# Optimization experiments

Hardware: AMD Instinct MI355X
Metric: run time of the kernel (lower is better)

## Reference

```python
import jax, jax.numpy as jnp
import numpy as np

B, S, H, NH, SPAN = 1, 2048, 768, 12, 512
D = H // NH
EPS = 1e-7
SCALE_FACTOR = 3  # 1 + len([c2p, p2c]) per DeBERTa


def setup_inputs() -> dict:
    key = jax.random.key(0)
    ks = jax.random.split(key, 10)
    r = lambda i, shape, s=0.02: jax.random.normal(ks[i], shape, jnp.float32) * s
    return dict(
        hidden_states=jax.random.normal(ks[0], (B, S, H), jnp.float32),
        attention_mask=jnp.ones((B, S), jnp.int32),
        Wq=r(1, (H, H)), bq=jnp.zeros((H,), jnp.float32),
        Wk=r(2, (H, H)), bk=jnp.zeros((H,), jnp.float32),
        Wv=r(3, (H, H)), bv=jnp.zeros((H,), jnp.float32),
        rel_embeddings=r(4, (2 * SPAN, H), 1.0),
        Wpk=r(5, (H, H)),
        Wpq=r(6, (H, H)), bpq=jnp.zeros((H,), jnp.float32),
        Wo=r(7, (H, H)), bo=jnp.zeros((H,), jnp.float32),
        ln_gamma=jnp.ones((H,), jnp.float32),
        ln_beta=jnp.zeros((H,), jnp.float32),
    )


def _heads(x):
    # [B,S,H] -> [B,NH,S,D]
    return x.reshape(B, S, NH, D).transpose(0, 2, 1, 3)


def reference(hidden_states, attention_mask, Wq, bq, Wk, bk, Wv, bv,
              rel_embeddings, Wpk, Wpq, bpq, Wo, bo, ln_gamma, ln_beta):
    q = _heads(hidden_states @ Wq + bq)
    k = _heads(hidden_states @ Wk + bk)
    v = _heads(hidden_states @ Wv + bv)
    scale = 1.0 / jnp.sqrt(jnp.asarray(D * SCALE_FACTOR, jnp.float32))

    # content-to-content
    scores = jnp.einsum('bhid,bhjd->bhij', q, k) * scale

    # relative positions: rel[i,j] = i - j
    ids = jnp.arange(S)
    rel = ids[:, None] - ids[None, :]                       # [S,S]

    pos_k = (rel_embeddings @ Wpk).reshape(2 * SPAN, NH, D)        # [2L,h,d]
    pos_q = (rel_embeddings @ Wpq + bpq).reshape(2 * SPAN, NH, D)  # [2L,h,d]

    # content-to-position: gather over clamped relative index
    c2p = jnp.einsum('bhid,lhd->bhil', q, pos_k) * scale    # [B,h,S,2L]
    c2p_idx = jnp.clip(rel + SPAN, 0, 2 * SPAN - 1)         # [S,S]
    c2p_att = c2p[:, :, ids[:, None], c2p_idx]              # [B,h,S,S]

    # position-to-content: gather then transpose (DeBERTa)
    p2c = jnp.einsum('bhjd,lhd->bhjl', k, pos_q) * scale    # [B,h,S,2L]
    p2c_idx = jnp.clip(-rel + SPAN, 0, 2 * SPAN - 1)        # [S,S]
    p2c_att = jnp.swapaxes(p2c[:, :, ids[:, None], p2c_idx], -1, -2)

    scores = scores + c2p_att + p2c_att

    mask4 = (attention_mask[:, None, None, :] * attention_mask[:, None, :, None]).astype(bool)
    scores = jnp.where(mask4, scores, jnp.finfo(scores.dtype).min)
    probs = jax.nn.softmax(scores, axis=-1)

    ctx = jnp.einsum('bhij,bhjd->bhid', probs, v).transpose(0, 2, 1, 3).reshape(B, S, H)

    # BertSelfOutput: dense + (dropout=identity) + residual + LayerNorm
    out = ctx @ Wo + bo + hidden_states
    mu = out.mean(-1, keepdims=True)
    var = out.var(-1, keepdims=True)
    return (out - mu) / jnp.sqrt(var + EPS) * ln_gamma + ln_beta
```

## Files before the change

### kernel.cpp

```cpp
#include <hip/hip_runtime.h>
#include <hip/hip_bf16.h>


typedef short v8s __attribute__((ext_vector_type(8)));
typedef short v4s __attribute__((ext_vector_type(4)));
typedef float v4f __attribute__((ext_vector_type(4)));

__device__ __forceinline__ float b2f(unsigned short u) {
    union { unsigned int i; float f; } v; v.i = ((unsigned int)u) << 16; return v.f;
}
__device__ __forceinline__ unsigned short f2b(float f) {
    union { float f; unsigned int i; } v; v.f = f;
    unsigned int x = v.i;
    return (unsigned short)((x + 0x7FFFu + ((x >> 16) & 1u)) >> 16);
}

#define SEQ 2048
#define HD  768
#define NH_ 12
#define DH  64

struct WtArgs { const float* src[6]; unsigned short* dst[6]; };
__global__ void prep_kernel(WtArgs args, const float* __restrict__ hs,
                            const float* __restrict__ rel,
                            const float* __restrict__ bq, const float* __restrict__ bk,
                            const float* __restrict__ bv, const float* __restrict__ bpq,
                            unsigned short* __restrict__ Xb, unsigned short* __restrict__ Rb,
                            float* __restrict__ bias3, float* __restrict__ bias2) {
    const int z = blockIdx.z;
    const int tx = threadIdx.x, ty = threadIdx.y;
    if (z < 6) {
        __shared__ float tile[32][33];
        const float* Sp = args.src[z];
        unsigned short* Dp = args.dst[z];
        const int bx = blockIdx.x * 32, by = blockIdx.y * 32;
#pragma unroll
        for (int r = 0; r < 32; r += 8) tile[ty + r][tx] = Sp[(by + ty + r) * HD + bx + tx];
        __syncthreads();
#pragma unroll
        for (int r = 0; r < 32; r += 8) Dp[(bx + ty + r) * HD + by + tx] = f2b(tile[tx][ty + r]);
    } else {
        const long n1 = (long)SEQ * HD;
        const long n2 = 1024l * HD;
        const long N = n1 + n2 + 3840;
        const long stride = 24l * 24 * 256;
        long i = ((long)blockIdx.y * 24 + blockIdx.x) * 256 + ty * 32 + tx;
        for (; i < N; i += stride) {
            if (i < n1) Xb[i] = f2b(hs[i]);
            else if (i < n1 + n2) Rb[i - n1] = f2b(rel[i - n1]);
            else {
                int j = (int)(i - n1 - n2);
                if (j < 768)        bias3[j] = bq[j];
                else if (j < 1536)  bias3[j] = bk[j - 768];
                else if (j < 2304)  bias3[j] = bv[j - 1536];
                else if (j < 3072)  bias2[j - 2304] = 0.0f;
                else                bias2[j - 2304] = bpq[j - 3072];
            }
        }
    }
}

template <int TM, int TN, int CTXA, int BIAS, int RESID, int OUTF32>
__device__ __forceinline__ void gemm_core(
    const unsigned short* __restrict__ A, int lda,
    const unsigned short* __restrict__ Bt, int ldb,
    void* __restrict__ Cv, int ldc,
    const float* __restrict__ bias, const float* __restrict__ resid,
    const float* __restrict__ opart, const float* __restrict__ lpart,
    int K, int m0, int n0, unsigned short* As, unsigned short* Bs) {
    constexpr int MT = TM / 32, NT = TN / 32;
    const int t = threadIdx.x;
    const int wave = t >> 6, lane = t & 63, quad = lane >> 4, l16 = lane & 15;
    const int wm = (wave & 1) * (TM / 2), wn = (wave >> 1) * (TN / 2);
    v4f acc[MT][NT];
    const v4f z4 = {0.f, 0.f, 0.f, 0.f};
#pragma unroll
    for (int i = 0; i < MT; i++)
#pragma unroll
        for (int j = 0; j < NT; j++) acc[i][j] = z4;

    const int arow = (TM == 128) ? (t >> 1) : (t >> 2);
    const int acol = (TM == 128) ? ((t & 1) * 32) : ((t & 3) * 16);
    const int brow = (TN == 128) ? (t >> 1) : (t >> 2);
    const int bcol = (TN == 128) ? ((t & 1) * 32) : ((t & 3) * 16);
    const unsigned short* ga = A + (long)(m0 + arow) * lda + acol;
    const unsigned short* gb = Bt + (long)(n0 + brow) * ldb + bcol;
    unsigned short* wa = &As[arow * 72 + acol];
    unsigned short* wb = &Bs[brow * 72 + bcol];

    for (int k0 = 0; k0 < K; k0 += 64) {
        __syncthreads();
        if constexpr (CTXA) {
            const int i = m0 + arow;
            const int h = k0 >> 6;
            float den = 0.f;
#pragma unroll
            for (int c = 0; c < 4; c++) den += lpart[((long)c * NH_ + h) * SEQ + i];
            const float inv = 1.0f / den;
            v8s pk0, pk1;
#pragma unroll
            for (int g = 0; g < 4; g++) {
                v4f s = z4;
#pragma unroll
                for (int c = 0; c < 4; c++)
                    s += *(const v4f*)(opart + (long)c * SEQ * HD + (long)i * HD + k0 + acol + g * 4);
#pragma unroll
                for (int u = 0; u < 4; u++) {
                    short v = (short)f2b(s[u] * inv);
                    if (g < 2) pk0[g * 4 + u] = v; else pk1[(g - 2) * 4 + u] = v;
                }
            }
            *(v8s*)wa = pk0; *(v8s*)(wa + 8) = pk1;
        } else if constexpr (TM == 128) {
            v8s a0 = *(const v8s*)(ga + k0);
            v8s a1 = *(const v8s*)(ga + k0 + 8);
            v8s a2 = *(const v8s*)(ga + k0 + 16);
            v8s a3 = *(const v8s*)(ga + k0 + 24);
            *(v8s*)(wa) = a0; *(v8s*)(wa + 8) = a1;
            *(v8s*)(wa + 16) = a2; *(v8s*)(wa + 24) = a3;
        } else {
            v8s a0 = *(const v8s*)(ga + k0);
            v8s a1 = *(const v8s*)(ga + k0 + 8);
            *(v8s*)(wa) = a0; *(v8s*)(wa + 8) = a1;
        }
        if constexpr (TN == 128) {
            v8s b0 = *(const v8s*)(gb + k0);
            v8s b1 = *(const v8s*)(gb + k0 + 8);
            v8s b2 = *(const v8s*)(gb + k0 + 16);
            v8s b3 = *(const v8s*)(gb + k0 + 24);
            *(v8s*)(wb) = b0; *(v8s*)(wb + 8) = b1;
            *(v8s*)(wb + 16) = b2; *(v8s*)(wb + 24) = b3;
        } else {
            v8s b0 = *(const v8s*)(gb + k0);
            v8s b1 = *(const v8s*)(gb + k0 + 8);
            *(v8s*)(wb) = b0; *(v8s*)(wb + 8) = b1;
        }
        __syncthreads();
#pragma unroll
        for (int ks = 0; ks < 2; ks++) {
            v8s af[MT], bf[NT];
#pragma unroll
            for (int mt = 0; mt < MT; mt++)
                af[mt] = *(const v8s*)&As[(wm + 16 * mt + l16) * 72 + ks * 32 + quad * 8];
#pragma unroll
            for (int nt = 0; nt < NT; nt++)
                bf[nt] = *(const v8s*)&Bs[(wn + 16 * nt + l16) * 72 + ks * 32 + quad * 8];
#pragma unroll
            for (int mt = 0; mt < MT; mt++)
#pragma unroll
                for (int nt = 0; nt < NT; nt++)
                    acc[mt][nt] = __builtin_amdgcn_mfma_f32_16x16x32_bf16(af[mt], bf[nt], acc[mt][nt], 0, 0, 0);
        }
    }
    float* Cf = (float*)Cv;
    unsigned short* Ch = (unsigned short*)Cv;
#pragma unroll
    for (int mt = 0; mt < MT; mt++) {
#pragma unroll
        for (int nt = 0; nt < NT; nt++) {
            const int gn = n0 + wn + 16 * nt + l16;
            float bv_ = 0.0f;
            if (BIAS) bv_ = bias[gn];
#pragma unroll
            for (int r = 0; r < 4; r++) {
                const int gm = m0 + wm + 16 * mt + quad * 4 + r;
                float v = acc[mt][nt][r];
                if (BIAS) v += bv_;
                if (RESID) v += resid[(long)gm * ldc + gn];
                if (OUTF32) Cf[(long)gm * ldc + gn] = v;
                else        Ch[(long)gm * ldc + gn] = f2b(v);
            }
        }
    }
}

__global__ __launch_bounds__(256) void gemm_qkvpos(
    const unsigned short* __restrict__ Xb, const unsigned short* __restrict__ Rb,
    const unsigned short* __restrict__ W3T, const unsigned short* __restrict__ Wp2T,
    const float* __restrict__ bias3, const float* __restrict__ bias2,
    unsigned short* __restrict__ qkv, unsigned short* __restrict__ pos2) {
    __shared__ unsigned short As[64 * 72];
    __shared__ unsigned short Bs[128 * 72];
    const int z = blockIdx.z;
    const int m0 = blockIdx.y * 64, n0 = blockIdx.x * 128;
    if (z < 3) {
        gemm_core<64, 128, 0, 1, 0, 0>(Xb, 768, W3T + (long)z * 768 * 768, 768,
                                       qkv + (long)z * 2048 * 768, 768, bias3 + z * 768,
                                       nullptr, nullptr, nullptr, 768, m0, n0, As, Bs);
    } else {
        if (blockIdx.y >= 16) return;
        const int w = z - 3;
        gemm_core<64, 128, 0, 1, 0, 0>(Rb, 768, Wp2T + (long)w * 768 * 768, 768,
                                       pos2 + (long)w * 1024 * 768, 768, bias2 + w * 768,
                                       nullptr, nullptr, nullptr, 768, m0, n0, As, Bs);
    }
}

__global__ __launch_bounds__(256) void gemm_band(
    const unsigned short* __restrict__ qkv, const unsigned short* __restrict__ pos2,
    unsigned short* __restrict__ c2p, unsigned short* __restrict__ p2c,
    const unsigned short* __restrict__ vsrc, unsigned short* __restrict__ vTs) {
    __shared__ unsigned short As[128 * 72];
    __shared__ unsigned short Bs[128 * 72];
    const int z = blockIdx.z;
    if (z < 24) {
        const unsigned short* A;
        const unsigned short* B;
        unsigned short* C;
        if (z < 12) {
            A = qkv + z * 64; B = pos2 + z * 64; C = c2p + (long)z * 2048 * 1024;
        } else {
            const int h = z - 12;
            A = qkv + 2048l * 768 + h * 64; B = pos2 + 1024l * 768 + h * 64;
            C = p2c + (long)h * 2048 * 1024;
        }
        gemm_core<128, 128, 0, 0, 0, 0>(A, 768, B, 768, C, 1024, nullptr, nullptr,
                                        nullptr, nullptr, 64,
                                        blockIdx.y * 128, blockIdx.x * 128, As, Bs);
    } else {
        unsigned short (*tile)[33] = (unsigned short(*)[33])As;
        const int b = blockIdx.y * 8 + blockIdx.x;
        const int tx = threadIdx.x & 31, ty = threadIdx.x >> 5;
        for (int tid = b; tid < 1536; tid += 128) {
            const int cx = (tid % 24) * 32;
            const int ry = (tid / 24) * 32;
            __syncthreads();
#pragma unroll
            for (int r = 0; r < 32; r += 8)
                tile[ty + r][tx] = vsrc[(long)(ry + ty + r) * HD + cx + tx];
            __syncthreads();
#pragma unroll
            for (int r = 0; r < 32; r += 8)
                vTs[(long)(cx + ty + r) * SEQ + ry + tx] = tile[tx][ty + r];
        }
    }
}

__global__ __launch_bounds__(256) void gemm_out(
    const float* __restrict__ opart, const float* __restrict__ lpart,
    const unsigned short* __restrict__ WoT,
    const float* __restrict__ bo, const float* __restrict__ hidden,
    float* __restrict__ out_pre) {
    __shared__ unsigned short As[64 * 72];
    __shared__ unsigned short Bs[64 * 72];
    gemm_core<64, 64, 1, 1, 1, 1>(nullptr, 768, WoT, 768, out_pre, 768, bo, hidden,
                                  opart, lpart, 768,
                                  blockIdx.y * 64, blockIdx.x * 64, As, Bs);
}

__device__ __forceinline__ void stage_window(const unsigned short* __restrict__ row,
                                             int D0, v8s& w0, v8s& w1) {
    if (D0 <= 0) {
        unsigned short v = row[0];
#pragma unroll
        for (int u = 0; u < 8; u++) { w0[u] = (short)v; w1[u] = (short)v; }
    } else if (D0 - 15 >= 1023) {
        unsigned short v = row[1023];
#pragma unroll
        for (int u = 0; u < 8; u++) { w0[u] = (short)v; w1[u] = (short)v; }
    } else if (D0 <= 1023 && D0 - 15 >= 0) {
        v8s x = *(const v8s*)(row + D0 - 7);
        v8s y = *(const v8s*)(row + D0 - 15);
#pragma unroll
        for (int u = 0; u < 8; u++) { w0[u] = x[7 - u]; w1[u] = y[7 - u]; }
    } else {
#pragma unroll
        for (int u = 0; u < 16; u++) {
            int d = D0 - u; d = d < 0 ? 0 : (d > 1023 ? 1023 : d);
            short v = (short)row[d];
            if (u < 8) w0[u] = v; else w1[u - 8] = v;
        }
    }
}

__global__ __launch_bounds__(256, 4) void flash_kernel(
    const unsigned short* __restrict__ qb, const unsigned short* __restrict__ kb,
    const unsigned short* __restrict__ vT, const unsigned short* __restrict__ c2p,
    const unsigned short* __restrict__ p2c, float* __restrict__ opart,
    float* __restrict__ lpart) {
    __shared__ unsigned short Kl[64 * 72];
    __shared__ unsigned short Vl[64 * 72];
    __shared__ unsigned short Pw[64 * 72];
    __shared__ unsigned short CwPl[64 * 72];
    const int h = blockIdx.y;
    const int i0 = blockIdx.x * 64;
    const int jc = blockIdx.z;
    const int jbase = jc * 512;
    const int t = threadIdx.x;
    const int wave = t >> 6, lane = t & 63, quad = lane >> 4, l16 = lane & 15;
    const float scale = 0.07216878364870322f;
    const v4f z4 = {0.f, 0.f, 0.f, 0.f};

    v8s qf[2];
    {
        const unsigned short* qp = qb + (long)(i0 + wave * 16 + l16) * HD + h * DH + quad * 8;
        qf[0] = *(const v8s*)qp;
        qf[1] = *(const v8s*)(qp + 32);
    }
    float l_lane[4] = {0.f, 0.f, 0.f, 0.f};
    v4f o_acc[4];
#pragma unroll
    for (int nt = 0; nt < 4; nt++) o_acc[nt] = z4;

    const int srow = t >> 2, scoff = (t & 3) * 16;
    const unsigned short* kbase = kb + (long)srow * HD + h * DH + scoff;
    const unsigned short* vbase = vT + (long)(h * DH + srow) * SEQ + scoff + jbase;
    unsigned short* wk = &Kl[srow * 72 + scoff];
    unsigned short* wv = &Vl[srow * 72 + scoff];
    unsigned short* wc = &CwPl[srow * 72 + scoff];
    unsigned short* wp = &Pw[srow * 72 + scoff];
    const unsigned short* c2prow = c2p + ((long)h * SEQ + i0 + srow) * 1024;
    const unsigned short* p2cb = p2c + (long)h * SEQ * 1024;

    v8s k0v, k1v, v0v, v1v, cw0, cw1, pw0, pw1;
    auto load_tile = [&](int j0l) {
        k0v = *(const v8s*)(kbase + (long)(jbase + j0l) * HD);
        k1v = *(const v8s*)(kbase + (long)(jbase + j0l) * HD + 8);
        v0v = *(const v8s*)(vbase + j0l);
        v1v = *(const v8s*)(vbase + j0l + 8);
        stage_window(c2prow, (i0 + srow) - (jbase + j0l) - scoff + 512, cw0, cw1);
        stage_window(p2cb + (long)(jbase + j0l + srow) * 1024,
                     (jbase + j0l + srow) - i0 - scoff + 512, pw0, pw1);
    };
    load_tile(0);

    for (int tt = 0; tt < 8; tt++) {
        __syncthreads();
        *(v8s*)wk = k0v; *(v8s*)(wk + 8) = k1v;
        *(v8s*)wv = v0v; *(v8s*)(wv + 8) = v1v;
        *(v8s*)wc = cw0; *(v8s*)(wc + 8) = cw1;
        *(v8s*)wp = pw0; *(v8s*)(wp + 8) = pw1;
        if (tt + 1 < 8) load_tile((tt + 1) * 64);
        __syncthreads();

        v4f s[4] = {z4, z4, z4, z4};
#pragma unroll
        for (int ks = 0; ks < 2; ks++)
#pragma unroll
            for (int nt = 0; nt < 4; nt++) {
                v8s bf = *(const v8s*)&Kl[(16 * nt + l16) * 72 + ks * 32 + quad * 8];
                s[nt] = __builtin_amdgcn_mfma_f32_16x16x32_bf16(qf[ks], bf, s[nt], 0, 0, 0);
            }
        float sm[4][4];
#pragma unroll
        for (int nt = 0; nt < 4; nt++) {
            v4s p4 = *(const v4s*)&Pw[(nt * 16 + l16) * 72 + wave * 16 + quad * 4];
#pragma unroll
            for (int r = 0; r < 4; r++) {
                float c2pv = b2f(CwPl[(wave * 16 + quad * 4 + r) * 72 + nt * 16 + l16]);
                float p = __expf((s[nt][r] + c2pv + b2f((unsigned short)p4[r])) * scale);
                sm[nt][r] = p;
                l_lane[r] += p;
            }
        }
#pragma unroll
        for (int nt = 0; nt < 4; nt++)
#pragma unroll
            for (int r = 0; r < 4; r++)
                CwPl[(wave * 16 + quad * 4 + r) * 72 + nt * 16 + l16] = f2b(sm[nt][r]);
        asm volatile("s_waitcnt lgkmcnt(0)" ::: "memory");
#pragma unroll
        for (int ks = 0; ks < 2; ks++) {
            v8s pf = *(const v8s*)&CwPl[(wave * 16 + l16) * 72 + ks * 32 + quad * 8];
#pragma unroll
            for (int nt = 0; nt < 4; nt++) {
                v8s vf = *(const v8s*)&Vl[(16 * nt + l16) * 72 + ks * 32 + quad * 8];
                o_acc[nt] = __builtin_amdgcn_mfma_f32_16x16x32_bf16(pf, vf, o_acc[nt], 0, 0, 0);
            }
        }
    }
    float* op = opart + (long)jc * SEQ * HD;
#pragma unroll
    for (int nt = 0; nt < 4; nt++) {
        const int d = nt * 16 + l16;
#pragma unroll
        for (int r = 0; r < 4; r++) {
            const int i = i0 + wave * 16 + quad * 4 + r;
            op[(long)i * HD + h * DH + d] = o_acc[nt][r];
        }
    }
#pragma unroll
    for (int r = 0; r < 4; r++) {
        float l = l_lane[r];
#pragma unroll
        for (int off = 1; off < 16; off <<= 1) l += __shfl_xor(l, off);
        l_lane[r] = l;
    }
    if (l16 == 0) {
#pragma unroll
        for (int r = 0; r < 4; r++) {
            const int i = i0 + wave * 16 + quad * 4 + r;
            lpart[((long)jc * NH_ + h) * SEQ + i] = l_lane[r];
        }
    }
}

__global__ __launch_bounds__(256) void ln_kernel(const float* __restrict__ x,
                                                 const float* __restrict__ gamma,
                                                 const float* __restrict__ beta,
                                                 float* __restrict__ out) {
    const int row = blockIdx.x;
    const int t = threadIdx.x;
    const float* xr = x + (long)row * HD;
    float v0 = xr[t], v1 = xr[t + 256], v2 = xr[t + 512];
    float s = v0 + v1 + v2;
    float ss = v0 * v0 + v1 * v1 + v2 * v2;
#pragma unroll
    for (int off = 1; off < 64; off <<= 1) { s += __shfl_xor(s, off); ss += __shfl_xor(ss, off); }
    __shared__ float red[8];
    const int wave = t >> 6;
    if ((t & 63) == 0) { red[wave] = s; red[wave + 4] = ss; }
    __syncthreads();
    float S = red[0] + red[1] + red[2] + red[3];
    float SS = red[4] + red[5] + red[6] + red[7];
    const float inv = 1.0f / 768.0f;
    float mu = S * inv;
    float var = SS * inv - mu * mu;
    float rstd = rsqrtf(var + 1e-7f);
    float* orow = out + (long)row * HD;
    orow[t]       = (v0 - mu) * rstd * gamma[t]       + beta[t];
    orow[t + 256] = (v1 - mu) * rstd * gamma[t + 256] + beta[t + 256];
    orow[t + 512] = (v2 - mu) * rstd * gamma[t + 512] + beta[t + 512];
}

extern "C" void kernel_launch(void* const* d_in, const int* in_sizes, int n_in,
                              void* d_out, int out_size, void* d_ws, size_t ws_size,
                              hipStream_t stream) {
    const float* hidden = (const float*)d_in[0];
    const float* Wq  = (const float*)d_in[2];
    const float* bq  = (const float*)d_in[3];
    const float* Wk  = (const float*)d_in[4];
    const float* bk  = (const float*)d_in[5];
    const float* Wv  = (const float*)d_in[6];
    const float* bv  = (const float*)d_in[7];
    const float* rel = (const float*)d_in[8];
    const float* Wpk = (const float*)d_in[9];
    const float* Wpq = (const float*)d_in[10];
    const float* bpq = (const float*)d_in[11];
    const float* Wo  = (const float*)d_in[12];
    const float* bo  = (const float*)d_in[13];
    const float* gamma = (const float*)d_in[14];
    const float* beta  = (const float*)d_in[15];

    char* ws = (char*)d_ws;
    size_t off = 0;
    auto alloc = [&](size_t bytes) -> char* { char* p = ws + off; off += bytes; return p; };
    unsigned short* Xb   = (unsigned short*)alloc(2048ul * 768 * 2);
    unsigned short* Rb   = (unsigned short*)alloc(1024ul * 768 * 2);
    unsigned short* W3T  = (unsigned short*)alloc(3ul * 768 * 768 * 2);
    unsigned short* WoT  = (unsigned short*)alloc(768ul * 768 * 2);
    unsigned short* Wp2T = (unsigned short*)alloc(2ul * 768 * 768 * 2);
    float*          bias3 = (float*)alloc(2304 * 4);
    float*          bias2 = (float*)alloc(1536 * 4);
    unsigned short* qkv  = (unsigned short*)alloc(3ul * 2048 * 768 * 2);
    unsigned short* vTs  = (unsigned short*)alloc(768ul * 2048 * 2);
    unsigned short* pos2 = (unsigned short*)alloc(2ul * 1024 * 768 * 2);
    unsigned short* c2p  = (unsigned short*)alloc(12ul * 2048 * 1024 * 2);
    unsigned short* p2c  = (unsigned short*)alloc(12ul * 2048 * 1024 * 2);
    float*          out_pre = (float*)alloc(2048ul * 768 * 4);
    float*          opart   = (float*)alloc(4ul * 2048 * 768 * 4);
    float*          lpart   = (float*)alloc(4ul * 12 * 2048 * 4);
    (void)ws_size;

    WtArgs wa;
    wa.src[0] = Wq;  wa.dst[0] = W3T;
    wa.src[1] = Wk;  wa.dst[1] = W3T + 768 * 768;
    wa.src[2] = Wv;  wa.dst[2] = W3T + 2 * 768 * 768;
    wa.src[3] = Wo;  wa.dst[3] = WoT;
    wa.src[4] = Wpk; wa.dst[4] = Wp2T;
    wa.src[5] = Wpq; wa.dst[5] = Wp2T + 768 * 768;
    prep_kernel<<<dim3(24, 24, 7), dim3(32, 8), 0, stream>>>(
        wa, hidden, rel, bq, bk, bv, bpq, Xb, Rb, bias3, bias2);

    gemm_qkvpos<<<dim3(6, 32, 5), 256, 0, stream>>>(Xb, Rb, W3T, Wp2T, bias3, bias2, qkv, pos2);
    gemm_band<<<dim3(8, 16, 25), 256, 0, stream>>>(qkv, pos2, c2p, p2c,
                                                   qkv + 2ul * 2048 * 768, vTs);
    flash_kernel<<<dim3(32, 12, 4), 256, 0, stream>>>(qkv, qkv + 2048ul * 768, vTs, c2p, p2c,
                                                      opart, lpart);
    gemm_out<<<dim3(12, 32), 256, 0, stream>>>(opart, lpart, WoT, bo, hidden, out_pre);
    ln_kernel<<<2048, 256, 0, stream>>>(out_pre, gamma, beta, (float*)d_out);
}
```

Measured before the change: 261.4 us.

## Fuse all stages into a persistent megakernel with software grid barriers

Replaces six separate kernel launches with one persistent kernel of 768 blocks that walks through each stage in a grid-stride loop and separates stages with an atomic-counter grid barrier. Flash partial outputs are now stored as bf16 instead of fp32, and the partial-sum combine moves into a separate elementwise pass that writes a bf16 ctx buffer for the output GEMM. The aim is to cut launch overhead, inter-kernel gaps and partial-output traffic. In exchange it relies on all 768 blocks being co-resident, since otherwise the barrier deadlocks, and it adds barrier latency plus some precision loss in the partials.

```diff
diff --git a/kernel.cpp b/kernel.cpp
--- a/kernel.cpp
+++ b/kernel.cpp
@@ -19,54 +19,44 @@
 #define HD  768
 #define NH_ 12
 #define DH  64
-
-struct WtArgs { const float* src[6]; unsigned short* dst[6]; };
-__global__ void prep_kernel(WtArgs args, const float* __restrict__ hs,
-                            const float* __restrict__ rel,
-                            const float* __restrict__ bq, const float* __restrict__ bk,
-                            const float* __restrict__ bv, const float* __restrict__ bpq,
-                            unsigned short* __restrict__ Xb, unsigned short* __restrict__ Rb,
-                            float* __restrict__ bias3, float* __restrict__ bias2) {
-    const int z = blockIdx.z;
-    const int tx = threadIdx.x, ty = threadIdx.y;
-    if (z < 6) {
-        __shared__ float tile[32][33];
-        const float* Sp = args.src[z];
-        unsigned short* Dp = args.dst[z];
-        const int bx = blockIdx.x * 32, by = blockIdx.y * 32;
-#pragma unroll
-        for (int r = 0; r < 32; r += 8) tile[ty + r][tx] = Sp[(by + ty + r) * HD + bx + tx];
-        __syncthreads();
-#pragma unroll
-        for (int r = 0; r < 32; r += 8) Dp[(bx + ty + r) * HD + by + tx] = f2b(tile[tx][ty + r]);
-    } else {
-        const long n1 = (long)SEQ * HD;
-        const long n2 = 1024l * HD;
-        const long N = n1 + n2 + 3840;
-        const long stride = 24l * 24 * 256;
-        long i = ((long)blockIdx.y * 24 + blockIdx.x) * 256 + ty * 32 + tx;
-        for (; i < N; i += stride) {
-            if (i < n1) Xb[i] = f2b(hs[i]);
-            else if (i < n1 + n2) Rb[i - n1] = f2b(rel[i - n1]);
-            else {
-                int j = (int)(i - n1 - n2);
-                if (j < 768)        bias3[j] = bq[j];
-                else if (j < 1536)  bias3[j] = bk[j - 768];
-                else if (j < 2304)  bias3[j] = bv[j - 1536];
-                else if (j < 3072)  bias2[j - 2304] = 0.0f;
-                else                bias2[j - 2304] = bpq[j - 3072];
-            }
-        }
-    }
-}
-
-template <int TM, int TN, int CTXA, int BIAS, int RESID, int OUTF32>
+#define NBLK 768
+
+struct MegaArgs {
+    const float *hs, *rel;
+    const float *Wq, *bq, *Wk, *bk, *Wv, *bv, *Wpk, *Wpq, *bpq, *Wo, *bo, *gamma, *beta;
+    unsigned short *Xb, *Rb, *W3T, *WoT, *Wp2T, *qkv, *vTs, *pos2, *c2p, *p2c, *ctx, *opart;
+    float *bias3, *bias2, *out_pre, *lpart, *outp;
+    unsigned* bar;
+};
+
+__device__ __forceinline__ void grid_sync(unsigned* bar) {
+    __syncthreads();
+    if (threadIdx.x == 0) {
+        unsigned* cnt = bar;
+        unsigned* gen = bar + 64;
+        unsigned g = __hip_atomic_load(gen, __ATOMIC_RELAXED, __HIP_MEMORY_SCOPE_AGENT);
+        unsigned a = __hip_atomic_fetch_add(cnt, 1u, __ATOMIC_ACQ_REL, __HIP_MEMORY_SCOPE_AGENT);
+        if (a == NBLK - 1) {
+            __hip_atomic_store(cnt, 0u, __ATOMIC_RELAXED, __HIP_MEMORY_SCOPE_AGENT);
+            __hip_atomic_store(gen, g + 1u, __ATOMIC_RELEASE, __HIP_MEMORY_SCOPE_AGENT);
+        } else {
+            unsigned cur;
+            do {
+                __builtin_amdgcn_s_sleep(16);
+                cur = __hip_atomic_load(gen, __ATOMIC_RELAXED, __HIP_MEMORY_SCOPE_AGENT);
+            } while (cur == g);
+            (void)__hip_atomic_load(gen, __ATOMIC_ACQUIRE, __HIP_MEMORY_SCOPE_AGENT);
+        }
+    }
+    __syncthreads();
+}
+
+template <int TM, int TN, int BIAS, int RESID, int OUTF32>
 __device__ __forceinline__ void gemm_core(
     const unsigned short* __restrict__ A, int lda,
     const unsigned short* __restrict__ Bt, int ldb,
     void* __restrict__ Cv, int ldc,
     const float* __restrict__ bias, const float* __restrict__ resid,
-    const float* __restrict__ opart, const float* __restrict__ lpart,
     int K, int m0, int n0, unsigned short* As, unsigned short* Bs) {
     constexpr int MT = TM / 32, NT = TN / 32;
     const int t = threadIdx.x;
@@ -90,28 +80,7 @@
 
     for (int k0 = 0; k0 < K; k0 += 64) {
         __syncthreads();
-        if constexpr (CTXA) {
-            const int i = m0 + arow;
-            const int h = k0 >> 6;
-            float den = 0.f;
-#pragma unroll
-            for (int c = 0; c < 4; c++) den += lpart[((long)c * NH_ + h) * SEQ + i];
-            const float inv = 1.0f / den;
-            v8s pk0, pk1;
-#pragma unroll
-            for (int g = 0; g < 4; g++) {
-                v4f s = z4;
-#pragma unroll
-                for (int c = 0; c < 4; c++)
-                    s += *(const v4f*)(opart + (long)c * SEQ * HD + (long)i * HD + k0 + acol + g * 4);
-#pragma unroll
-                for (int u = 0; u < 4; u++) {
-                    short v = (short)f2b(s[u] * inv);
-                    if (g < 2) pk0[g * 4 + u] = v; else pk1[(g - 2) * 4 + u] = v;
-                }
-            }
-            *(v8s*)wa = pk0; *(v8s*)(wa + 8) = pk1;
-        } else if constexpr (TM == 128) {
+        if constexpr (TM == 128) {
             v8s a0 = *(const v8s*)(ga + k0);
             v8s a1 = *(const v8s*)(ga + k0 + 8);
             v8s a2 = *(const v8s*)(ga + k0 + 16);
@@ -174,80 +143,6 @@
     }
 }
 
-__global__ __launch_bounds__(256) void gemm_qkvpos(
-    const unsigned short* __restrict__ Xb, const unsigned short* __restrict__ Rb,
-    const unsigned short* __restrict__ W3T, const unsigned short* __restrict__ Wp2T,
-    const float* __restrict__ bias3, const float* __restrict__ bias2,
-    unsigned short* __restrict__ qkv, unsigned short* __restrict__ pos2) {
-    __shared__ unsigned short As[64 * 72];
-    __shared__ unsigned short Bs[128 * 72];
-    const int z = blockIdx.z;
-    const int m0 = blockIdx.y * 64, n0 = blockIdx.x * 128;
-    if (z < 3) {
-        gemm_core<64, 128, 0, 1, 0, 0>(Xb, 768, W3T + (long)z * 768 * 768, 768,
-                                       qkv + (long)z * 2048 * 768, 768, bias3 + z * 768,
-                                       nullptr, nullptr, nullptr, 768, m0, n0, As, Bs);
-    } else {
-        if (blockIdx.y >= 16) return;
-        const int w = z - 3;
-        gemm_core<64, 128, 0, 1, 0, 0>(Rb, 768, Wp2T + (long)w * 768 * 768, 768,
-                                       pos2 + (long)w * 1024 * 768, 768, bias2 + w * 768,
-                                       nullptr, nullptr, nullptr, 768, m0, n0, As, Bs);
-    }
-}
-
-__global__ __launch_bounds__(256) void gemm_band(
-    const unsigned short* __restrict__ qkv, const unsigned short* __restrict__ pos2,
-    unsigned short* __restrict__ c2p, unsigned short* __restrict__ p2c,
-    const unsigned short* __restrict__ vsrc, unsigned short* __restrict__ vTs) {
-    __shared__ unsigned short As[128 * 72];
-    __shared__ unsigned short Bs[128 * 72];
-    const int z = blockIdx.z;
-    if (z < 24) {
-        const unsigned short* A;
-        const unsigned short* B;
-        unsigned short* C;
-        if (z < 12) {
-            A = qkv + z * 64; B = pos2 + z * 64; C = c2p + (long)z * 2048 * 1024;
-        } else {
-            const int h = z - 12;
-            A = qkv + 2048l * 768 + h * 64; B = pos2 + 1024l * 768 + h * 64;
-            C = p2c + (long)h * 2048 * 1024;
-        }
-        gemm_core<128, 128, 0, 0, 0, 0>(A, 768, B, 768, C, 1024, nullptr, nullptr,
-                                        nullptr, nullptr, 64,
-                                        blockIdx.y * 128, blockIdx.x * 128, As, Bs);
-    } else {
-        unsigned short (*tile)[33] = (unsigned short(*)[33])As;
-        const int b = blockIdx.y * 8 + blockIdx.x;
-        const int tx = threadIdx.x & 31, ty = threadIdx.x >> 5;
-        for (int tid = b; tid < 1536; tid += 128) {
-            const int cx = (tid % 24) * 32;
-            const int ry = (tid / 24) * 32;
-            __syncthreads();
-#pragma unroll
-            for (int r = 0; r < 32; r += 8)
-                tile[ty + r][tx] = vsrc[(long)(ry + ty + r) * HD + cx + tx];
-            __syncthreads();
-#pragma unroll
-            for (int r = 0; r < 32; r += 8)
-                vTs[(long)(cx + ty + r) * SEQ + ry + tx] = tile[tx][ty + r];
-        }
-    }
-}
-
-__global__ __launch_bounds__(256) void gemm_out(
-    const float* __restrict__ opart, const float* __restrict__ lpart,
-    const unsigned short* __restrict__ WoT,
-    const float* __restrict__ bo, const float* __restrict__ hidden,
-    float* __restrict__ out_pre) {
-    __shared__ unsigned short As[64 * 72];
-    __shared__ unsigned short Bs[64 * 72];
-    gemm_core<64, 64, 1, 1, 1, 1>(nullptr, 768, WoT, 768, out_pre, 768, bo, hidden,
-                                  opart, lpart, 768,
-                                  blockIdx.y * 64, blockIdx.x * 64, As, Bs);
-}
-
 __device__ __forceinline__ void stage_window(const unsigned short* __restrict__ row,
                                              int D0, v8s& w0, v8s& w1) {
     if (D0 <= 0) {
@@ -273,23 +168,19 @@
     }
 }
 
-__global__ __launch_bounds__(256, 4) void flash_kernel(
-    const unsigned short* __restrict__ qb, const unsigned short* __restrict__ kb,
-    const unsigned short* __restrict__ vT, const unsigned short* __restrict__ c2p,
-    const unsigned short* __restrict__ p2c, float* __restrict__ opart,
-    float* __restrict__ lpart) {
-    __shared__ unsigned short Kl[64 * 72];
-    __shared__ unsigned short Vl[64 * 72];
-    __shared__ unsigned short Pw[64 * 72];
-    __shared__ unsigned short CwPl[64 * 72];
-    const int h = blockIdx.y;
-    const int i0 = blockIdx.x * 64;
-    const int jc = blockIdx.z;
+__device__ __forceinline__ void flash_unit(const MegaArgs& a, int i0, int h, int jc,
+                                           unsigned short* smem) {
+    unsigned short* Kl = smem;
+    unsigned short* Vl = smem + 4608;
+    unsigned short* Pw = smem + 9216;
+    unsigned short* CwPl = smem + 13824;
     const int jbase = jc * 512;
     const int t = threadIdx.x;
     const int wave = t >> 6, lane = t & 63, quad = lane >> 4, l16 = lane & 15;
     const float scale = 0.07216878364870322f;
     const v4f z4 = {0.f, 0.f, 0.f, 0.f};
+    const unsigned short* qb = a.qkv;
+    const unsigned short* kb = a.qkv + (long)SEQ * HD;
 
     v8s qf[2];
     {
@@ -304,13 +195,13 @@
 
     const int srow = t >> 2, scoff = (t & 3) * 16;
     const unsigned short* kbase = kb + (long)srow * HD + h * DH + scoff;
-    const unsigned short* vbase = vT + (long)(h * DH + srow) * SEQ + scoff + jbase;
+    const unsigned short* vbase = a.vTs + (long)(h * DH + srow) * SEQ + scoff + jbase;
     unsigned short* wk = &Kl[srow * 72 + scoff];
     unsigned short* wv = &Vl[srow * 72 + scoff];
     unsigned short* wc = &CwPl[srow * 72 + scoff];
     unsigned short* wp = &Pw[srow * 72 + scoff];
-    const unsigned short* c2prow = c2p + ((long)h * SEQ + i0 + srow) * 1024;
-    const unsigned short* p2cb = p2c + (long)h * SEQ * 1024;
+    const unsigned short* c2prow = a.c2p + ((long)h * SEQ + i0 + srow) * 1024;
+    const unsigned short* p2cb = a.p2c + (long)h * SEQ * 1024;
 
     v8s k0v, k1v, v0v, v1v, cw0, cw1, pw0, pw1;
     auto load_tile = [&](int j0l) {
@@ -369,14 +260,14 @@
             }
         }
     }
-    float* op = opart + (long)jc * SEQ * HD;
+    unsigned short* op = a.opart + (long)jc * SEQ * HD;
 #pragma unroll
     for (int nt = 0; nt < 4; nt++) {
         const int d = nt * 16 + l16;
 #pragma unroll
         for (int r = 0; r < 4; r++) {
             const int i = i0 + wave * 16 + quad * 4 + r;
-            op[(long)i * HD + h * DH + d] = o_acc[nt][r];
+            op[(long)i * HD + h * DH + d] = f2b(o_acc[nt][r]);
         }
     }
 #pragma unroll
@@ -390,93 +281,216 @@
 #pragma unroll
         for (int r = 0; r < 4; r++) {
             const int i = i0 + wave * 16 + quad * 4 + r;
-            lpart[((long)jc * NH_ + h) * SEQ + i] = l_lane[r];
-        }
-    }
-}
-
-__global__ __launch_bounds__(256) void ln_kernel(const float* __restrict__ x,
-                                                 const float* __restrict__ gamma,
-                                                 const float* __restrict__ beta,
-                                                 float* __restrict__ out) {
-    const int row = blockIdx.x;
+            a.lpart[((long)jc * NH_ + h) * SEQ + i] = l_lane[r];
+        }
+    }
+}
+
+__global__ __launch_bounds__(256, 4) void mega_kernel(MegaArgs a) {
+    __shared__ unsigned short smem[18432];
+    const int bid = blockIdx.x;
     const int t = threadIdx.x;
-    const float* xr = x + (long)row * HD;
-    float v0 = xr[t], v1 = xr[t + 256], v2 = xr[t + 512];
-    float s = v0 + v1 + v2;
-    float ss = v0 * v0 + v1 * v1 + v2 * v2;
-#pragma unroll
-    for (int off = 1; off < 64; off <<= 1) { s += __shfl_xor(s, off); ss += __shfl_xor(ss, off); }
-    __shared__ float red[8];
-    const int wave = t >> 6;
-    if ((t & 63) == 0) { red[wave] = s; red[wave + 4] = ss; }
-    __syncthreads();
-    float S = red[0] + red[1] + red[2] + red[3];
-    float SS = red[4] + red[5] + red[6] + red[7];
-    const float inv = 1.0f / 768.0f;
-    float mu = S * inv;
-    float var = SS * inv - mu * mu;
-    float rstd = rsqrtf(var + 1e-7f);
-    float* orow = out + (long)row * HD;
-    orow[t]       = (v0 - mu) * rstd * gamma[t]       + beta[t];
-    orow[t + 256] = (v1 - mu) * rstd * gamma[t + 256] + beta[t + 256];
-    orow[t + 512] = (v2 - mu) * rstd * gamma[t + 512] + beta[t + 512];
+
+    {
+        const float* wsrc[6] = {a.Wq, a.Wk, a.Wv, a.Wo, a.Wpk, a.Wpq};
+        unsigned short* wdst[6] = {a.W3T, a.W3T + 768 * 768, a.W3T + 2 * 768 * 768,
+                                   a.WoT, a.Wp2T, a.Wp2T + 768 * 768};
+        float (*tile)[33] = (float(*)[33])smem;
+        const int tx = t & 31, ty = t >> 5;
+        for (int u = bid; u < 3456 + NBLK; u += NBLK) {
+            if (u < 3456) {
+                const int z = u / 576, rem = u % 576;
+                const int by = (rem / 24) * 32, bx = (rem % 24) * 32;
+                const float* Sp = wsrc[z];
+                unsigned short* Dp = wdst[z];
+                __syncthreads();
+#pragma unroll
+                for (int r = 0; r < 32; r += 8) tile[ty + r][tx] = Sp[(by + ty + r) * HD + bx + tx];
+                __syncthreads();
+#pragma unroll
+                for (int r = 0; r < 32; r += 8) Dp[(bx + ty + r) * HD + by + tx] = f2b(tile[tx][ty + r]);
+            } else {
+                const int v = u - 3456;
+                const long n1 = (long)SEQ * HD;
+                const long n2 = 1024l * HD;
+                const long N = n1 + n2 + 3840;
+                for (long i = (long)v * 256 + t; i < N; i += (long)NBLK * 256) {
+                    if (i < n1) a.Xb[i] = f2b(a.hs[i]);
+                    else if (i < n1 + n2) a.Rb[i - n1] = f2b(a.rel[i - n1]);
+                    else {
+                        int j = (int)(i - n1 - n2);
+                        if (j < 768)        a.bias3[j] = a.bq[j];
+                        else if (j < 1536)  a.bias3[j] = a.bk[j - 768];
+                        else if (j < 2304)  a.bias3[j] = a.bv[j - 1536];
+                        else if (j < 3072)  a.bias2[j - 2304] = 0.0f;
+                        else                a.bias2[j - 2304] = a.bpq[j - 3072];
+                    }
+                }
+            }
+        }
+    }
+    grid_sync(a.bar);
+
+    {
+        unsigned short* As = smem;
+        unsigned short* Bs = smem + 64 * 72;
+        for (int u = bid; u < 768; u += NBLK) {
+            if (u < 576) {
+                const int z = u / 192, rem = u % 192;
+                const int m0 = (rem / 6) * 64, n0 = (rem % 6) * 128;
+                gemm_core<64, 128, 1, 0, 0>(a.Xb, 768, a.W3T + (long)z * 768 * 768, 768,
+                                            a.qkv + (long)z * SEQ * HD, 768,
+                                            a.bias3 + z * 768, nullptr, 768, m0, n0, As, Bs);
+            } else {
+                const int v = u - 576;
+                const int w = v / 96, rem = v % 96;
+                const int m0 = (rem / 6) * 64, n0 = (rem % 6) * 128;
+                gemm_core<64, 128, 1, 0, 0>(a.Rb, 768, a.Wp2T + (long)w * 768 * 768, 768,
+                                            a.pos2 + (long)w * 1024 * 768, 768,
+                                            a.bias2 + w * 768, nullptr, 768, m0, n0, As, Bs);
+            }
+        }
+    }
+    grid_sync(a.bar);
+
+    {
+        unsigned short* As = smem;
+        unsigned short* Bs = smem + 128 * 72;
+        for (int u = bid; u < 3072 + 1536; u += NBLK) {
+            if (u < 3072) {
+                const int z = u >> 7, rem = u & 127;
+                const int m0 = (rem >> 3) * 128, n0 = (rem & 7) * 128;
+                const unsigned short *A, *B;
+                unsigned short* C;
+                if (z < 12) {
+                    A = a.qkv + z * 64; B = a.pos2 + z * 64; C = a.c2p + (long)z * SEQ * 1024;
+                } else {
+                    const int h = z - 12;
+                    A = a.qkv + (long)SEQ * HD + h * 64;
+                    B = a.pos2 + 1024l * 768 + h * 64;
+                    C = a.p2c + (long)h * SEQ * 1024;
+                }
+                gemm_core<128, 128, 0, 0, 0>(A, 768, B, 768, C, 1024, nullptr, nullptr,
+                                             64, m0, n0, As, Bs);
+            } else {
+                const int v = u - 3072;
+                unsigned short (*tile)[33] = (unsigned short(*)[33])smem;
+                const unsigned short* vsrc = a.qkv + 2l * SEQ * HD;
+                const int tx = t & 31, ty = t >> 5;
+                const int cx = (v % 24) * 32, ry = (v / 24) * 32;
+                __syncthreads();
+#pragma unroll
+                for (int r = 0; r < 32; r += 8)
+                    tile[ty + r][tx] = vsrc[(long)(ry + ty + r) * HD + cx + tx];
+                __syncthreads();
+#pragma unroll
+                for (int r = 0; r < 32; r += 8)
+                    a.vTs[(long)(cx + ty + r) * SEQ + ry + tx] = tile[tx][ty + r];
+            }
+        }
+    }
+    grid_sync(a.bar);
+
+    for (int u = bid; u < 1536; u += NBLK) {
+        const int i0 = (u & 31) * 64;
+        const int h = (u >> 5) % 12;
+        const int jc = u / 384;
+        flash_unit(a, i0, h, jc, smem);
+    }
+    grid_sync(a.bar);
+
+    for (long idx = (long)bid * 256 + t; idx < (long)SEQ * HD; idx += (long)NBLK * 256) {
+        const int i = (int)(idx / HD);
+        const int h = ((int)(idx % HD)) >> 6;
+        float num = 0.f, den = 0.f;
+#pragma unroll
+        for (int c = 0; c < 4; c++) {
+            num += b2f(a.opart[(long)c * SEQ * HD + idx]);
+            den += a.lpart[((long)c * NH_ + h) * SEQ + i];
+        }
+        a.ctx[idx] = f2b(num / den);
+    }
+    grid_sync(a.bar);
+
+    {
+        unsigned short* As = smem;
+        unsigned short* Bs = smem + 64 * 72;
+        for (int u = bid; u < 384; u += NBLK) {
+            const int m0 = (u / 12) * 64, n0 = (u % 12) * 64;
+            gemm_core<64, 64, 1, 1, 1>(a.ctx, 768, a.WoT, 768, a.out_pre, 768,
+                                       a.bo, a.hs, 768, m0, n0, As, Bs);
+        }
+    }
+    grid_sync(a.bar);
+
+    {
+        float* red = (float*)smem;
+        const int wave = t >> 6;
+        for (int row = bid; row < SEQ; row += NBLK) {
+            __syncthreads();
+            const float* xr = a.out_pre + (long)row * HD;
+            float v0 = xr[t], v1 = xr[t + 256], v2 = xr[t + 512];
+            float s = v0 + v1 + v2;
+            float ss = v0 * v0 + v1 * v1 + v2 * v2;
+#pragma unroll
+            for (int off = 1; off < 64; off <<= 1) {
+                s += __shfl_xor(s, off); ss += __shfl_xor(ss, off);
+            }
+            if ((t & 63) == 0) { red[wave] = s; red[wave + 4] = ss; }
+            __syncthreads();
+            float S = red[0] + red[1] + red[2] + red[3];
+            float SS = red[4] + red[5] + red[6] + red[7];
+            const float inv = 1.0f / 768.0f;
+            float mu = S * inv;
+            float var = SS * inv - mu * mu;
+            float rstd = rsqrtf(var + 1e-7f);
+            float* orow = a.outp + (long)row * HD;
+            orow[t]       = (v0 - mu) * rstd * a.gamma[t]       + a.beta[t];
+            orow[t + 256] = (v1 - mu) * rstd * a.gamma[t + 256] + a.beta[t + 256];
+            orow[t + 512] = (v2 - mu) * rstd * a.gamma[t + 512] + a.beta[t + 512];
+        }
+    }
 }
 
 extern "C" void kernel_launch(void* const* d_in, const int* in_sizes, int n_in,
                               void* d_out, int out_size, void* d_ws, size_t ws_size,
                               hipStream_t stream) {
-    const float* hidden = (const float*)d_in[0];
-    const float* Wq  = (const float*)d_in[2];
-    const float* bq  = (const float*)d_in[3];
-    const float* Wk  = (const float*)d_in[4];
-    const float* bk  = (const float*)d_in[5];
-    const float* Wv  = (const float*)d_in[6];
-    const float* bv  = (const float*)d_in[7];
-    const float* rel = (const float*)d_in[8];
-    const float* Wpk = (const float*)d_in[9];
-    const float* Wpq = (const float*)d_in[10];
-    const float* bpq = (const float*)d_in[11];
-    const float* Wo  = (const float*)d_in[12];
-    const float* bo  = (const float*)d_in[13];
-    const float* gamma = (const float*)d_in[14];
-    const float* beta  = (const float*)d_in[15];
-
     char* ws = (char*)d_ws;
-    size_t off = 0;
+    size_t off = 512;
     auto alloc = [&](size_t bytes) -> char* { char* p = ws + off; off += bytes; return p; };
-    unsigned short* Xb   = (unsigned short*)alloc(2048ul * 768 * 2);
-    unsigned short* Rb   = (unsigned short*)alloc(1024ul * 768 * 2);
-    unsigned short* W3T  = (unsigned short*)alloc(3ul * 768 * 768 * 2);
-    unsigned short* WoT  = (unsigned short*)alloc(768ul * 768 * 2);
-    unsigned short* Wp2T = (unsigned short*)alloc(2ul * 768 * 768 * 2);
-    float*          bias3 = (float*)alloc(2304 * 4);
-    float*          bias2 = (float*)alloc(1536 * 4);
-    unsigned short* qkv  = (unsigned short*)alloc(3ul * 2048 * 768 * 2);
-    unsigned short* vTs  = (unsigned short*)alloc(768ul * 2048 * 2);
-    unsigned short* pos2 = (unsigned short*)alloc(2ul * 1024 * 768 * 2);
-    unsigned short* c2p  = (unsigned short*)alloc(12ul * 2048 * 1024 * 2);
-    unsigned short* p2c  = (unsigned short*)alloc(12ul * 2048 * 1024 * 2);
-    float*          out_pre = (float*)alloc(2048ul * 768 * 4);
-    float*          opart   = (float*)alloc(4ul * 2048 * 768 * 4);
-    float*          lpart   = (float*)alloc(4ul * 12 * 2048 * 4);
+
+    MegaArgs a;
+    a.hs  = (const float*)d_in[0];
+    a.Wq  = (const float*)d_in[2];  a.bq  = (const float*)d_in[3];
+    a.Wk  = (const float*)d_in[4];  a.bk  = (const float*)d_in[5];
+    a.Wv  = (const float*)d_in[6];  a.bv  = (const float*)d_in[7];
+    a.rel = (const float*)d_in[8];
+    a.Wpk = (const float*)d_in[9];  a.Wpq = (const float*)d_in[10];
+    a.bpq = (const float*)d_in[11];
+    a.Wo  = (const float*)d_in[12]; a.bo  = (const float*)d_in[13];
+    a.gamma = (const float*)d_in[14];
+    a.beta  = (const float*)d_in[15];
+
+    a.Xb   = (unsigned short*)alloc(2048ul * 768 * 2);
+    a.Rb   = (unsigned short*)alloc(1024ul * 768 * 2);
+    a.W3T  = (unsigned short*)alloc(3ul * 768 * 768 * 2);
+    a.WoT  = (unsigned short*)alloc(768ul * 768 * 2);
+    a.Wp2T = (unsigned short*)alloc(2ul * 768 * 768 * 2);
+    a.bias3 = (float*)alloc(2304 * 4);
+    a.bias2 = (float*)alloc(1536 * 4);
+    a.qkv  = (unsigned short*)alloc(3ul * 2048 * 768 * 2);
+    a.vTs  = (unsigned short*)alloc(768ul * 2048 * 2);
+    a.pos2 = (unsigned short*)alloc(2ul * 1024 * 768 * 2);
+    a.c2p  = (unsigned short*)alloc(12ul * 2048 * 1024 * 2);
+    a.p2c  = (unsigned short*)alloc(12ul * 2048 * 1024 * 2);
+    a.ctx  = (unsigned short*)alloc(2048ul * 768 * 2);
+    a.opart = (unsigned short*)alloc(4ul * 2048 * 768 * 2);
+    a.out_pre = (float*)alloc(2048ul * 768 * 4);
+    a.lpart   = (float*)alloc(4ul * 12 * 2048 * 4);
+    a.outp = (float*)d_out;
+    a.bar  = (unsigned*)d_ws;
     (void)ws_size;
 
-    WtArgs wa;
-    wa.src[0] = Wq;  wa.dst[0] = W3T;
-    wa.src[1] = Wk;  wa.dst[1] = W3T + 768 * 768;
-    wa.src[2] = Wv;  wa.dst[2] = W3T + 2 * 768 * 768;
-    wa.src[3] = Wo;  wa.dst[3] = WoT;
-    wa.src[4] = Wpk; wa.dst[4] = Wp2T;
-    wa.src[5] = Wpq; wa.dst[5] = Wp2T + 768 * 768;
-    prep_kernel<<<dim3(24, 24, 7), dim3(32, 8), 0, stream>>>(
-        wa, hidden, rel, bq, bk, bv, bpq, Xb, Rb, bias3, bias2);
-
-    gemm_qkvpos<<<dim3(6, 32, 5), 256, 0, stream>>>(Xb, Rb, W3T, Wp2T, bias3, bias2, qkv, pos2);
-    gemm_band<<<dim3(8, 16, 25), 256, 0, stream>>>(qkv, pos2, c2p, p2c,
-                                                   qkv + 2ul * 2048 * 768, vTs);
-    flash_kernel<<<dim3(32, 12, 4), 256, 0, stream>>>(qkv, qkv + 2048ul * 768, vTs, c2p, p2c,
-                                                      opart, lpart);
-    gemm_out<<<dim3(12, 32), 256, 0, stream>>>(opart, lpart, WoT, bo, hidden, out_pre);
-    ln_kernel<<<2048, 256, 0, stream>>>(out_pre, gamma, beta, (float*)d_out);
-}
+    hipMemsetAsync(d_ws, 0, 512, stream);
+    mega_kernel<<<NBLK, 256, 0, stream>>>(a);
+}
```

New measurement: 416.0 us. +59.2%, slower.
